# Optimization experiments

Hardware: AMD Instinct MI355X
Metric: run time of the kernel (lower is better)

## Reference

```python
import jax, jax.numpy as jnp
import numpy as np

DIM = 1024; HEADS = 16; DH = DIM // HEADS
BLOCK = 64; NSEL = 8
B = 1; N = 2048
CD = BLOCK * DH   # compress_dim
HID = CD          # mlp_expansion = 1


def setup_inputs():
    key = jax.random.key(0)
    ks = jax.random.split(key, 12)
    def nrm(k, shape, scale=0.02):
        return jax.random.normal(k, shape, dtype=jnp.float32) * scale
    x = jax.random.normal(ks[0], (B, N, DIM), dtype=jnp.float32)
    inv = 1.0 / (10000.0 ** (np.arange(0, DH, 2, dtype=np.float32) / DH))
    ang = np.arange(N, dtype=np.float32)[:, None] * inv[None, :]
    freqs_cis = jnp.asarray(np.stack([np.cos(ang), np.sin(ang)], axis=-1))  # [N, DH/2, 2]
    return {
        'x': x, 'freqs_cis': freqs_cis,
        'Wq': nrm(ks[1], (DIM, DIM)), 'Wk': nrm(ks[2], (DIM, DIM)),
        'Wv': nrm(ks[3], (DIM, DIM)), 'Wo': nrm(ks[4], (DIM, DIM)),
        'pe': nrm(ks[5], (BLOCK, HEADS, DH)),
        'kW1': nrm(ks[6], (CD, HID)), 'kb1': jnp.zeros((HID,), jnp.float32),
        'kW2': nrm(ks[7], (HID, DH)), 'kb2': jnp.zeros((DH,), jnp.float32),
        'vW1': nrm(ks[8], (CD, HID)), 'vb1': jnp.zeros((HID,), jnp.float32),
        'vW2': nrm(ks[9], (HID, DH)), 'vb2': jnp.zeros((DH,), jnp.float32),
        'Wc': nrm(ks[10], (DIM, 2 * HEADS)), 'bc': jnp.zeros((2 * HEADS,), jnp.float32),
    }


def _rope(t, cos, sin):
    # t: [b,n,h,d]; rotate consecutive pairs by per-position angles
    t2 = t.reshape(t.shape[:-1] + (DH // 2, 2))
    tr, ti = t2[..., 0], t2[..., 1]
    c = cos[None, :, None, :]
    s = sin[None, :, None, :]
    out = jnp.stack([tr * c - ti * s, tr * s + ti * c], axis=-1)
    return out.reshape(t.shape)


def reference(x, freqs_cis, Wq, Wk, Wv, Wo, pe, kW1, kb1, kW2, kb2, vW1, vb1, vW2, vb2, Wc, bc):
    b, n, _ = x.shape
    w = n // BLOCK
    scale = DH ** -0.5
    q = (x @ Wq).reshape(b, n, HEADS, DH)
    k = (x @ Wk).reshape(b, n, HEADS, DH)
    v = (x @ Wv).reshape(b, n, HEADS, DH)
    # intra-block PE added only on the compression branch
    kb = k.reshape(b, w, BLOCK, HEADS, DH) + pe[None, None]
    vb = v.reshape(b, w, BLOCK, HEADS, DH) + pe[None, None]

    def compress(blocks, W1, b1, W2, b2):
        h = blocks.transpose(0, 1, 3, 2, 4).reshape(b, w, HEADS, CD)  # b w h (n d)
        h = jax.nn.relu(h @ W1 + b1)
        return h @ W2 + b2  # [b,w,h,dh]

    ck = compress(kb, kW1, kb1, kW2, kb2)
    cv = compress(vb, vW1, vb1, vW2, vb2)
    # compressed attention (no rope on q here, matching the source)
    cscore = jax.nn.softmax(jnp.einsum('bqhd,bkhd->bhqk', q, ck) * scale, axis=-1)  # [b,h,n,w]
    compressed = jnp.einsum('bhqk,bkhd->bqhd', cscore, cv)

    cos, sin = freqs_cis[..., 0], freqs_cis[..., 1]
    sq = _rope(q, cos, sin)
    sk = _rope(k, cos, sin)

    nsel = min(NSEL, w)
    idx = jax.lax.top_k(cscore, nsel)[1]  # [b,h,n,nsel] selected block ids per query
    # dense qk scores, then per-query block gather == gathered sparse attention
    sf = (jnp.einsum('bqhd,bkhd->bhqk', sq, sk) * scale).reshape(b, HEADS, n, w, BLOCK)
    sel = jnp.take_along_axis(sf, idx[..., None], axis=3)  # [b,h,n,nsel,BLOCK]
    probs = jax.nn.softmax(sel.reshape(b, HEADS, n, nsel * BLOCK), axis=-1)
    probs = probs.reshape(b, HEADS, n, nsel, BLOCK)
    # scatter selected-softmax back to full key axis (topk ids are distinct)
    onehot = (idx[..., None] == jnp.arange(w)).astype(probs.dtype)  # [b,h,n,nsel,w]
    full = jnp.einsum('bhqsn,bhqsw->bhqwn', probs, onehot).reshape(b, HEADS, n, n)
    selected = jnp.einsum('bhqk,bkhd->bqhd', full, v)  # sv = v without PE

    gate = jax.nn.sigmoid(x @ Wc + bc).reshape(b, n, 2, HEADS)  # b n (s h) -> b n s h
    y = jnp.einsum('bnsh,sbnhd->bnhd', gate, jnp.stack([compressed, selected]))
    return y.reshape(b, n, DIM) @ Wo
```

## Files before the change

kernel.cpp:

```cpp
#include <hip/hip_runtime.h>
#include <hip/hip_bf16.h>

#define N_TOK   2048
#define DIM     1024
#define HEADS   16
#define DH      64
#define WBLK    32
#define NSEL    8
#define CD      4096

typedef __hip_bfloat16 bf16;
typedef __attribute__((ext_vector_type(8))) short short8;
typedef __attribute__((ext_vector_type(4))) float f32x4;

__device__ __forceinline__ void gll16(const void* g, void* l) {
    __builtin_amdgcn_global_load_lds((const __attribute__((address_space(1))) void*)g,
                                     (__attribute__((address_space(3))) void*)l, 16, 0, 0);
}

template<int PAIRS, int OUT>
__global__ __launch_bounds__(256, 2) void gemm_mfma(
    const bf16* __restrict__ a0, const bf16* __restrict__ a1, const bf16* __restrict__ a2,
    const bf16* __restrict__ b0, const bf16* __restrict__ b1, const bf16* __restrict__ b2,
    const float* __restrict__ bias, float* __restrict__ C,
    bf16* __restrict__ C0, bf16* __restrict__ C1,
    int M, int N, int K, int act)
{
    constexpr int NS = (PAIRS == 6) ? 3 : ((PAIRS >= 3) ? 2 : 1);
    __shared__ __align__(16) bf16 As[3][NS][64][32];
    __shared__ __align__(16) bf16 Bs[3][NS][64][32];

    const int tid = threadIdx.x, lane = tid & 63, wid = tid >> 6;
    const int wr = wid >> 1, wc = wid & 1;
    const int row0 = blockIdx.y * 64, col0 = blockIdx.x * 64;

    const bf16* ap[3] = {a0, a1, a2};
    const bf16* bp[3] = {b0, b1, b2};

    f32x4 acc[2][2];
    #pragma unroll
    for (int mi = 0; mi < 2; ++mi)
        #pragma unroll
        for (int ni = 0; ni < 2; ++ni) acc[mi][ni] = (f32x4){0.f, 0.f, 0.f, 0.f};

    const int lr = lane >> 2;
    const int lc = (((lane & 3) ^ ((lane >> 3) & 3))) * 8;
    const int fo = (((lane >> 4) ^ ((lane >> 1) & 3))) * 8;

    constexpr int pa[6] = {0, 0, 1, 1, 0, 2};
    constexpr int pb[6] = {0, 1, 0, 1, 2, 0};

    auto stage = [&](int buf, int t) {
        const int k0 = t << 5;
        #pragma unroll
        for (int s = 0; s < NS; ++s) {
            gll16(ap[s] + (size_t)(row0 + wid * 16 + lr) * K + k0 + lc, &As[buf][s][wid * 16][0]);
            gll16(bp[s] + (size_t)(col0 + wid * 16 + lr) * K + k0 + lc, &Bs[buf][s][wid * 16][0]);
        }
    };

    const int nt = K >> 5;
    stage(0, 0);
    if (nt > 1) {
        stage(1, 1);
        asm volatile("s_waitcnt vmcnt(%0)" :: "n"(2 * NS) : "memory");
    } else {
        asm volatile("s_waitcnt vmcnt(0)" ::: "memory");
    }
    __builtin_amdgcn_s_barrier();

    for (int t = 0; t < nt; ++t) {
        const int cur = t % 3;

        short8 af[2][NS], bfr[2][NS];
        #pragma unroll
        for (int mi = 0; mi < 2; ++mi)
            #pragma unroll
            for (int s = 0; s < NS; ++s)
                af[mi][s] = *(const short8*)&As[cur][s][wr * 32 + mi * 16 + (lane & 15)][fo];
        #pragma unroll
        for (int ni = 0; ni < 2; ++ni)
            #pragma unroll
            for (int s = 0; s < NS; ++s)
                bfr[ni][s] = *(const short8*)&Bs[cur][s][wc * 32 + ni * 16 + (lane & 15)][fo];

        if (t + 2 < nt) stage((t + 2) % 3, t + 2);

        #pragma unroll
        for (int mi = 0; mi < 2; ++mi)
            #pragma unroll
            for (int ni = 0; ni < 2; ++ni) {
                f32x4 c = acc[mi][ni];
                #pragma unroll
                for (int p = 0; p < PAIRS; ++p)
                    c = __builtin_amdgcn_mfma_f32_16x16x32_bf16(af[mi][pa[p]], bfr[ni][pb[p]], c, 0, 0, 0);
                acc[mi][ni] = c;
            }

        if (t + 1 < nt) {
            if (t + 2 < nt) asm volatile("s_waitcnt vmcnt(%0)" :: "n"(2 * NS) : "memory");
            else            asm volatile("s_waitcnt vmcnt(0)" ::: "memory");
            __builtin_amdgcn_s_barrier();
        }
    }

    #pragma unroll
    for (int mi = 0; mi < 2; ++mi)
        #pragma unroll
        for (int ni = 0; ni < 2; ++ni)
            #pragma unroll
            for (int r = 0; r < 4; ++r) {
                int row = row0 + wr * 32 + mi * 16 + (lane >> 4) * 4 + r;
                int col = col0 + wc * 32 + ni * 16 + (lane & 15);
                float v = acc[mi][ni][r];
                if (bias) v += bias[col];
                if (act == 1) v = fmaxf(v, 0.f);
                if (OUT == 0 || OUT == 3) C[(size_t)row * N + col] = v;
                if (OUT == 2 || OUT == 3) {
                    bf16 hh = __float2bfloat16(v);
                    C0[(size_t)row * N + col] = hh;
                    C1[(size_t)row * N + col] = __float2bfloat16(v - __bfloat162float(hh));
                }
            }
}

template<int KC>
__global__ __launch_bounds__(256, 2) void sk_gemm(
    const bf16* __restrict__ a0, const bf16* __restrict__ a1,
    const bf16* __restrict__ b0, const bf16* __restrict__ b1,
    float* __restrict__ part, int M, int K)
{
    __shared__ __align__(16) bf16 As[3][2][64][32];
    __shared__ __align__(16) bf16 Bs[3][2][64][32];
    const int tid = threadIdx.x, lane = tid & 63, wid = tid >> 6;
    const int wr = wid >> 1, wc = wid & 1;
    const int row0 = blockIdx.x * 64;
    const int kchunk = K / KC;
    const int kbase = blockIdx.y * kchunk;
    const bf16* ap[2] = {a0, a1};
    const bf16* bp[2] = {b0, b1};
    const int lr = lane >> 2;
    const int lc = (((lane & 3) ^ ((lane >> 3) & 3))) * 8;
    const int fo = (((lane >> 4) ^ ((lane >> 1) & 3))) * 8;

    f32x4 acc[2][2];
    #pragma unroll
    for (int mi = 0; mi < 2; ++mi)
        #pragma unroll
        for (int ni = 0; ni < 2; ++ni) acc[mi][ni] = (f32x4){0.f, 0.f, 0.f, 0.f};

    auto stage = [&](int buf, int t) {
        const int k0 = kbase + (t << 5);
        #pragma unroll
        for (int s = 0; s < 2; ++s) {
            gll16(ap[s] + (size_t)(row0 + wid * 16 + lr) * K + k0 + lc, &As[buf][s][wid * 16][0]);
            gll16(bp[s] + (size_t)(wid * 16 + lr) * K + k0 + lc,        &Bs[buf][s][wid * 16][0]);
        }
    };

    const int nt = kchunk >> 5;
    stage(0, 0);
    if (nt > 1) {
        stage(1, 1);
        asm volatile("s_waitcnt vmcnt(4)" ::: "memory");
    } else {
        asm volatile("s_waitcnt vmcnt(0)" ::: "memory");
    }
    __builtin_amdgcn_s_barrier();

    for (int t = 0; t < nt; ++t) {
        const int cur = t % 3;
        short8 af[2][2], bfr[2][2];
        #pragma unroll
        for (int mi = 0; mi < 2; ++mi)
            #pragma unroll
            for (int s = 0; s < 2; ++s)
                af[mi][s] = *(const short8*)&As[cur][s][wr * 32 + mi * 16 + (lane & 15)][fo];
        #pragma unroll
        for (int ni = 0; ni < 2; ++ni)
            #pragma unroll
            for (int s = 0; s < 2; ++s)
                bfr[ni][s] = *(const short8*)&Bs[cur][s][wc * 32 + ni * 16 + (lane & 15)][fo];

        if (t + 2 < nt) stage((t + 2) % 3, t + 2);

        #pragma unroll
        for (int mi = 0; mi < 2; ++mi)
            #pragma unroll
            for (int ni = 0; ni < 2; ++ni) {
                f32x4 c = acc[mi][ni];
                c = __builtin_amdgcn_mfma_f32_16x16x32_bf16(af[mi][0], bfr[ni][0], c, 0, 0, 0);
                c = __builtin_amdgcn_mfma_f32_16x16x32_bf16(af[mi][0], bfr[ni][1], c, 0, 0, 0);
                c = __builtin_amdgcn_mfma_f32_16x16x32_bf16(af[mi][1], bfr[ni][0], c, 0, 0, 0);
                acc[mi][ni] = c;
            }

        if (t + 1 < nt) {
            if (t + 2 < nt) asm volatile("s_waitcnt vmcnt(4)" ::: "memory");
            else            asm volatile("s_waitcnt vmcnt(0)" ::: "memory");
            __builtin_amdgcn_s_barrier();
        }
    }

    #pragma unroll
    for (int mi = 0; mi < 2; ++mi)
        #pragma unroll
        for (int ni = 0; ni < 2; ++ni)
            #pragma unroll
            for (int r = 0; r < 4; ++r) {
                int row = row0 + wr * 32 + mi * 16 + (lane >> 4) * 4 + r;
                int col = wc * 32 + ni * 16 + (lane & 15);
                part[((size_t)blockIdx.y * M + row) * 64 + col] = acc[mi][ni][r];
            }
}

__global__ void skred(const float* __restrict__ part, const float* __restrict__ bias,
                      float* __restrict__ C, bf16* __restrict__ C0, bf16* __restrict__ C1,
                      int M, int KC) {
    int i = blockIdx.x * 256 + threadIdx.x;
    if (i >= M * 64) return;
    float s = bias ? bias[i & 63] : 0.f;
    for (int kc = 0; kc < KC; ++kc) s += part[(size_t)kc * M * 64 + i];
    C[i] = s;
    if (C0) {
        bf16 hh = __float2bfloat16(s);
        C0[i] = hh;
        C1[i] = __float2bfloat16(s - __bfloat162float(hh));
    }
}

__global__ __launch_bounds__(256) void cscore_gemm(const bf16* __restrict__ qs0,
                                                   const bf16* __restrict__ qs1,
                                                   const bf16* __restrict__ ck0,
                                                   const bf16* __restrict__ ck1,
                                                   float* __restrict__ Sc) {
    int h = blockIdx.y;
    int wid = threadIdx.x >> 6, lane = threadIdx.x & 63;
    int q0 = blockIdx.x * 128 + wid * 32;
    const int lr = lane & 15, hc = lane >> 4;

    f32x4 acc[2][2];
    #pragma unroll
    for (int a = 0; a < 2; ++a)
        #pragma unroll
        for (int b = 0; b < 2; ++b) acc[a][b] = (f32x4){0.f, 0.f, 0.f, 0.f};

    short8 av[2][2][2], bv[2][2][2];
    #pragma unroll
    for (int qs_ = 0; qs_ < 2; ++qs_)
        #pragma unroll
        for (int ks = 0; ks < 2; ++ks) {
            size_t off = ((size_t)(q0 + qs_ * 16 + lr) << 10) + (h << 6) + ks * 32 + hc * 8;
            av[qs_][ks][0] = *(const short8*)(qs0 + off);
            av[qs_][ks][1] = *(const short8*)(qs1 + off);
        }
    #pragma unroll
    for (int ws = 0; ws < 2; ++ws)
        #pragma unroll
        for (int ks = 0; ks < 2; ++ks) {
            size_t off = ((size_t)(((ws * 16 + lr) << 4) + h)) * 64 + ks * 32 + hc * 8;
            bv[ws][ks][0] = *(const short8*)(ck0 + off);
            bv[ws][ks][1] = *(const short8*)(ck1 + off);
        }
    #pragma unroll
    for (int qs_ = 0; qs_ < 2; ++qs_)
        #pragma unroll
        for (int ws = 0; ws < 2; ++ws) {
            f32x4 c = acc[qs_][ws];
            #pragma unroll
            for (int ks = 0; ks < 2; ++ks) {
                c = __builtin_amdgcn_mfma_f32_16x16x32_bf16(av[qs_][ks][0], bv[ws][ks][0], c, 0, 0, 0);
                c = __builtin_amdgcn_mfma_f32_16x16x32_bf16(av[qs_][ks][0], bv[ws][ks][1], c, 0, 0, 0);
                c = __builtin_amdgcn_mfma_f32_16x16x32_bf16(av[qs_][ks][1], bv[ws][ks][0], c, 0, 0, 0);
            }
            acc[qs_][ws] = c;
        }
    #pragma unroll
    for (int qs_ = 0; qs_ < 2; ++qs_)
        #pragma unroll
        for (int ws = 0; ws < 2; ++ws)
            #pragma unroll
            for (int r = 0; r < 4; ++r) {
                int q = q0 + qs_ * 16 + hc * 4 + r;
                int w = ws * 16 + lr;
                Sc[((size_t)(h << 11) + q) * 32 + w] = acc[qs_][ws][r] * 0.125f;
            }
}

__global__ __launch_bounds__(256) void ctopk_pv(const float* __restrict__ Sc,
                                                const float* __restrict__ cv,
                                                float* __restrict__ comp,
                                                int* __restrict__ idxb) {
    int item = blockIdx.x * 4 + (threadIdx.x >> 6);
    int lane = threadIdx.x & 63;
    int h = item >> 11, qpos = item & 2047;
    float logit = (lane < 32) ? Sc[(size_t)item * 32 + lane] : -1e30f;
    float m = logit;
    #pragma unroll
    for (int o = 32; o; o >>= 1) m = fmaxf(m, __shfl_xor(m, o));
    float e = (lane < 32) ? expf(logit - m) : 0.f;
    float s = e;
    #pragma unroll
    for (int o = 32; o; o >>= 1) s += __shfl_xor(s, o);
    float inv = 1.f / s;
    float acc = 0.f;
    #pragma unroll 8
    for (int w = 0; w < WBLK; ++w) {
        float pw = __shfl(e, w) * inv;
        acc += pw * cv[(size_t)((w << 4) + h) * 64 + lane];
    }
    comp[(size_t)(qpos << 10) + (h << 6) + lane] = acc;
    int rank = 0;
    #pragma unroll 8
    for (int j = 0; j < WBLK; ++j) {
        float lj = __shfl(logit, j);
        rank += (lj > logit || (lj == logit && j < lane)) ? 1 : 0;
    }
    if (lane < 32 && rank < NSEL) idxb[item * NSEL + rank] = lane;
}

__global__ __launch_bounds__(256) void gate_gemm(const float* __restrict__ x,
                                                 const float* __restrict__ Wc,
                                                 const float* __restrict__ bc,
                                                 float* __restrict__ gate) {
    __shared__ float xr[1024];
    __shared__ float part[8][32];
    int row = blockIdx.x;
    #pragma unroll
    for (int i = 0; i < 4; ++i)
        xr[threadIdx.x + i * 256] = x[(size_t)row * 1024 + threadIdx.x + i * 256];
    __syncthreads();
    int c = threadIdx.x & 31, sl = threadIdx.x >> 5;
    float acc = 0.f;
    for (int k = sl; k < 1024; k += 8) acc += xr[k] * Wc[k * 32 + c];
    part[sl][c] = acc;
    __syncthreads();
    if (sl == 0) {
        float v = bc[c];
        #pragma unroll
        for (int j = 0; j < 8; ++j) v += part[j][c];
        gate[(size_t)row * 32 + c] = 1.f / (1.f + expf(-v));
    }
}

template<int NS>
__global__ __launch_bounds__(256) void tsplit(const float* __restrict__ B,
                                              bf16* __restrict__ t0, bf16* __restrict__ t1,
                                              bf16* __restrict__ t2, int K, int N) {
    __shared__ float tile[32][33];
    int tx = threadIdx.x & 31, ty = threadIdx.x >> 5;
    int bx = blockIdx.x, by = blockIdx.y;
    #pragma unroll
    for (int i = 0; i < 4; ++i)
        tile[ty + i * 8][tx] = B[(size_t)(by * 32 + ty + i * 8) * N + bx * 32 + tx];
    __syncthreads();
    #pragma unroll
    for (int i = 0; i < 4; ++i) {
        int nn = bx * 32 + ty + i * 8;
        int kk = by * 32 + tx;
        float x = tile[tx][ty + i * 8];
        bf16 h = __float2bfloat16(x);
        t0[(size_t)nn * K + kk] = h;
        if (NS >= 2) {
            float r1 = x - __bfloat162float(h);
            bf16 m = __float2bfloat16(r1);
            t1[(size_t)nn * K + kk] = m;
            if (NS == 3) t2[(size_t)nn * K + kk] = __float2bfloat16(r1 - __bfloat162float(m));
        }
    }
}

__global__ void split2_k(const float* __restrict__ s, bf16* __restrict__ d0,
                         bf16* __restrict__ d1, int n) {
    int i = blockIdx.x * 256 + threadIdx.x;
    if (i >= n) return;
    float x = s[i];
    bf16 h = __float2bfloat16(x); d0[i] = h;
    d1[i] = __float2bfloat16(x - __bfloat162float(h));
}

__global__ void build_cmat2(const float* __restrict__ kv, const float* __restrict__ pe,
                            bf16* __restrict__ c0, bf16* __restrict__ c1) {
    int i = blockIdx.x * 256 + threadIdx.x;
    int r = i >> 12, c = i & 4095;
    int w = r >> 4, h = r & 15;
    int pos = c >> 6, d = c & 63;
    float x = kv[(size_t)((w * 64 + pos) << 10) + (h << 6) + d] +
              pe[(size_t)((pos << 4) + h) * 64 + d];
    bf16 hh = __float2bfloat16(x); c0[i] = hh;
    c1[i] = __float2bfloat16(x - __bfloat162float(hh));
}
__global__ void build_cmat1(const float* __restrict__ kv, const float* __restrict__ pe,
                            bf16* __restrict__ c0) {
    int i = blockIdx.x * 256 + threadIdx.x;
    int r = i >> 12, c = i & 4095;
    int w = r >> 4, h = r & 15;
    int pos = c >> 6, d = c & 63;
    float x = kv[(size_t)((w * 64 + pos) << 10) + (h << 6) + d] +
              pe[(size_t)((pos << 4) + h) * 64 + d];
    c0[i] = __float2bfloat16(x);
}
__global__ void build_cmat(const float* __restrict__ kv, const float* __restrict__ pe,
                           float* __restrict__ cmat) {
    int i = blockIdx.x * 256 + threadIdx.x;
    int r = i >> 12, c = i & 4095;
    int w = r >> 4, h = r & 15;
    int pos = c >> 6, d = c & 63;
    cmat[i] = kv[(size_t)((w * 64 + pos) << 10) + (h << 6) + d] +
              pe[(size_t)((pos << 4) + h) * 64 + d];
}

__global__ __launch_bounds__(256) void gemm_skinny64(const float* __restrict__ A,
                                                     const float* __restrict__ B,
                                                     const float* __restrict__ bias,
                                                     float* __restrict__ C, int K) {
    __shared__ float Arow[4096];
    __shared__ float part[4][64];
    int row = blockIdx.x;
    for (int i = threadIdx.x; i < K; i += 256) Arow[i] = A[(size_t)row * K + i];
    __syncthreads();
    int c = threadIdx.x & 63, sl = threadIdx.x >> 6;
    float acc = 0.f;
    for (int k = sl; k < K; k += 4) acc += Arow[k] * B[(size_t)k * 64 + c];
    part[sl][c] = acc;
    __syncthreads();
    if (sl == 0) {
        float v = part[0][c] + part[1][c] + part[2][c] + part[3][c];
        if (bias) v += bias[c];
        C[(size_t)row * 64 + c] = v;
    }
}

__global__ __launch_bounds__(256) void gemm_f32(const float* __restrict__ A,
                                                const float* __restrict__ B,
                                                const float* __restrict__ bias,
                                                float* __restrict__ C,
                                                int M, int N, int K, int act) {
    __shared__ float As[16][65];
    __shared__ float Bs[16][65];
    const int tid  = threadIdx.x;
    const int row0 = blockIdx.y * 64;
    const int col0 = blockIdx.x * 64;
    const int tm = tid >> 4;
    const int tn = tid & 15;

    float acc[4][4];
    #pragma unroll
    for (int i = 0; i < 4; ++i)
        #pragma unroll
        for (int j = 0; j < 4; ++j) acc[i][j] = 0.f;

    const int ar  = tid >> 2;
    const int akq = (tid & 3) << 2;

    for (int k0 = 0; k0 < K; k0 += 16) {
        float4 a4 = make_float4(0.f, 0.f, 0.f, 0.f);
        if (row0 + ar < M)
            a4 = *reinterpret_cast<const float4*>(&A[(size_t)(row0 + ar) * K + k0 + akq]);
        As[akq + 0][ar] = a4.x; As[akq + 1][ar] = a4.y;
        As[akq + 2][ar] = a4.z; As[akq + 3][ar] = a4.w;
        #pragma unroll
        for (int it = 0; it < 4; ++it) {
            int idx = tid + it * 256;
            int kr = idx >> 6, c = idx & 63;
            float bv = 0.f;
            if (col0 + c < N) bv = B[(size_t)(k0 + kr) * N + col0 + c];
            Bs[kr][c] = bv;
        }
        __syncthreads();
        #pragma unroll
        for (int kk = 0; kk < 16; ++kk) {
            float a0 = As[kk][tm * 4 + 0], a1 = As[kk][tm * 4 + 1];
            float a2 = As[kk][tm * 4 + 2], a3 = As[kk][tm * 4 + 3];
            float b0v = Bs[kk][tn * 4 + 0], b1v = Bs[kk][tn * 4 + 1];
            float b2v = Bs[kk][tn * 4 + 2], b3v = Bs[kk][tn * 4 + 3];
            acc[0][0] += a0 * b0v; acc[0][1] += a0 * b1v; acc[0][2] += a0 * b2v; acc[0][3] += a0 * b3v;
            acc[1][0] += a1 * b0v; acc[1][1] += a1 * b1v; acc[1][2] += a1 * b2v; acc[1][3] += a1 * b3v;
            acc[2][0] += a2 * b0v; acc[2][1] += a2 * b1v; acc[2][2] += a2 * b2v; acc[2][3] += a2 * b3v;
            acc[3][0] += a3 * b0v; acc[3][1] += a3 * b1v; acc[3][2] += a3 * b2v; acc[3][3] += a3 * b3v;
        }
        __syncthreads();
    }

    #pragma unroll
    for (int i = 0; i < 4; ++i) {
        int r = row0 + tm * 4 + i;
        if (r >= M) continue;
        #pragma unroll
        for (int j = 0; j < 4; ++j) {
            int cc = col0 + tn * 4 + j;
            if (cc >= N) continue;
            float vv = acc[i][j];
            if (bias) vv += bias[cc];
            if (act == 1) vv = fmaxf(vv, 0.f);
            else if (act == 2) vv = 1.f / (1.f + expf(-vv));
            C[(size_t)r * N + cc] = vv;
        }
    }
}

__global__ __launch_bounds__(256) void cscore_topk(const float* __restrict__ q,
                                                   const float* __restrict__ ck,
                                                   float* __restrict__ cprob,
                                                   int* __restrict__ idxb) {
    int item = blockIdx.x * 4 + (threadIdx.x >> 6);
    int lane = threadIdx.x & 63;
    int h = item >> 11;
    int qpos = item & 2047;
    float qv = q[(size_t)(qpos << 10) + (h << 6) + lane];
    float logit = -1e30f;
    const float scale = 0.125f;
    for (int w = 0; w < WBLK; ++w) {
        float p = qv * ck[(size_t)((w << 4) + h) * 64 + lane];
        #pragma unroll
        for (int o = 32; o; o >>= 1) p += __shfl_xor(p, o);
        if (lane == w) logit = p * scale;
    }
    float m = logit;
    #pragma unroll
    for (int o = 32; o; o >>= 1) m = fmaxf(m, __shfl_xor(m, o));
    float e = (lane < 32) ? expf(logit - m) : 0.f;
    float s = e;
    #pragma unroll
    for (int o = 32; o; o >>= 1) s += __shfl_xor(s, o);
    if (lane < 32) cprob[(size_t)item * WBLK + lane] = e / s;
    float vcur = logit;
    for (int t = 0; t < NSEL; ++t) {
        float bm = vcur; int bi = lane;
        #pragma unroll
        for (int o = 32; o; o >>= 1) {
            float om = __shfl_xor(bm, o); int oi = __shfl_xor(bi, o);
            if (om > bm || (om == bm && oi < bi)) { bm = om; bi = oi; }
        }
        if (lane == 0) idxb[item * NSEL + t] = bi;
        if (lane == bi) vcur = -1e30f;
    }
}
__global__ void compressed_pv(const float* __restrict__ cprob, const float* __restrict__ cv,
                              float* __restrict__ comp) {
    int i = blockIdx.x * 256 + threadIdx.x;
    int qpos = i >> 10; int hd = i & 1023; int h = hd >> 6; int d = hd & 63;
    const float* pr = &cprob[(size_t)(h * N_TOK + qpos) * WBLK];
    float acc = 0.f;
    #pragma unroll
    for (int w = 0; w < WBLK; ++w) acc += pr[w] * cv[(size_t)((w << 4) + h) * 64 + d];
    comp[i] = acc;
}

__global__ void rope_ip(float* __restrict__ q, float* __restrict__ k,
                        const float* __restrict__ fc) {
    int i = blockIdx.x * 256 + threadIdx.x;
    int n = i >> 9; int hp = i & 511; int h = hp >> 5; int p = hp & 31;
    float c = fc[(size_t)(n * 32 + p) * 2];
    float s = fc[(size_t)(n * 32 + p) * 2 + 1];
    size_t base = (size_t)(n << 10) + (h << 6) + (p << 1);
    float qr = q[base], qi = q[base + 1];
    q[base] = qr * c - qi * s; q[base + 1] = qr * s + qi * c;
    float kr = k[base], ki = k[base + 1];
    k[base] = kr * c - ki * s; k[base + 1] = kr * s + ki * c;
}

__global__ void rope_convert_qk(const float* __restrict__ q, const float* __restrict__ k,
                                const float* __restrict__ fc,
                                bf16* __restrict__ qb, bf16* __restrict__ kb) {
    int i = blockIdx.x * 256 + threadIdx.x;
    int n = i >> 9; int hp = i & 511; int h = hp >> 5; int p = hp & 31;
    float c = fc[(size_t)(n * 32 + p) * 2];
    float s = fc[(size_t)(n * 32 + p) * 2 + 1];
    size_t base = (size_t)(n << 10) + (h << 6) + (p << 1);
    float qr = q[base], qi = q[base + 1];
    qb[base]     = __float2bfloat16(0.125f * (qr * c - qi * s));
    qb[base + 1] = __float2bfloat16(0.125f * (qr * s + qi * c));
    float kr = k[base], ki = k[base + 1];
    kb[base]     = __float2bfloat16(kr * c - ki * s);
    kb[base + 1] = __float2bfloat16(kr * s + ki * c);
}

__global__ __launch_bounds__(256) void convert_vT(const float* __restrict__ v,
                                                  bf16* __restrict__ vbT) {
    __shared__ float tile[64][65];
    int h = blockIdx.x;
    int n0 = blockIdx.y * 64;
    int tx = threadIdx.x & 63, ty = threadIdx.x >> 6;
    #pragma unroll
    for (int i = 0; i < 16; ++i)
        tile[ty + 4 * i][tx] = v[(size_t)(n0 + ty + 4 * i) * 1024 + (h << 6) + tx];
    __syncthreads();
    #pragma unroll
    for (int i = 0; i < 16; ++i) {
        int d = ty + 4 * i;
        vbT[((size_t)(h << 6) + d) * 2048 + n0 + tx] = __float2bfloat16(tile[tx][d]);
    }
}

__global__ void zero_counts(int* __restrict__ counts) { counts[threadIdx.x] = 0; }

__global__ void build_lists(const int* __restrict__ idxb, int* __restrict__ counts,
                            int* __restrict__ lists) {
    int i = blockIdx.x * 256 + threadIdx.x;
    int item = i >> 3, t = i & 7;
    int h = item >> 11, q = item & 2047;
    int w = idxb[i];
    int g = h * 32 + w;
    int pos = atomicAdd(&counts[g], 1);
    lists[g * 2048 + pos] = (q << 3) | t;
}

__global__ void convert_qkv(const float* __restrict__ q, const float* __restrict__ k,
                            const float* __restrict__ v, bf16* __restrict__ qb,
                            bf16* __restrict__ kb, bf16* __restrict__ vbT) {
    int i = blockIdx.x * 256 + threadIdx.x;
    qb[i] = __float2bfloat16(0.125f * q[i]);
    kb[i] = __float2bfloat16(k[i]);
    int h = i >> 17, d = (i >> 11) & 63, n = i & 2047;
    vbT[i] = __float2bfloat16(v[(size_t)(n << 10) + (h << 6) + d]);
}

__global__ __launch_bounds__(64) void sel_scores(const bf16* __restrict__ qb,
                                                 const bf16* __restrict__ kb,
                                                 const int* __restrict__ counts,
                                                 const int* __restrict__ lists,
                                                 float* __restrict__ S) {
    int g = blockIdx.x;
    int cnt = counts[g];
    int tile = blockIdx.y;
    if (tile * 32 >= cnt) return;
    int h = g >> 5, w = g & 31;
    int lane = threadIdx.x;
    __shared__ int qt[32];
    __shared__ float st[32][66];
    int nrow = cnt - tile * 32; if (nrow > 32) nrow = 32;
    if (lane < 32) qt[lane] = lists[g * 2048 + tile * 32 + (lane < nrow ? lane : nrow - 1)];
    __syncthreads();
    int lr = lane & 15, hc = lane >> 4;

    f32x4 acc[2][4];
    #pragma unroll
    for (int m = 0; m < 2; ++m)
        #pragma unroll
        for (int gk = 0; gk < 4; ++gk) acc[m][gk] = (f32x4){0.f, 0.f, 0.f, 0.f};

    short8 a[2][2], b[4][2];
    #pragma unroll
    for (int m = 0; m < 2; ++m) {
        int qq = qt[m * 16 + lr] >> 3;
        const bf16* ar = qb + ((size_t)qq << 10) + (h << 6) + hc * 8;
        a[m][0] = *(const short8*)ar;
        a[m][1] = *(const short8*)(ar + 32);
    }
    #pragma unroll
    for (int gk = 0; gk < 4; ++gk) {
        const bf16* kr = kb + ((size_t)((w << 6) + gk * 16 + lr) << 10) + (h << 6) + hc * 8;
        b[gk][0] = *(const short8*)kr;
        b[gk][1] = *(const short8*)(kr + 32);
    }
    #pragma unroll
    for (int m = 0; m < 2; ++m)
        #pragma unroll
        for (int gk = 0; gk < 4; ++gk) {
            acc[m][gk] = __builtin_amdgcn_mfma_f32_16x16x32_bf16(a[m][0], b[gk][0], acc[m][gk], 0, 0, 0);
            acc[m][gk] = __builtin_amdgcn_mfma_f32_16x16x32_bf16(a[m][1], b[gk][1], acc[m][gk], 0, 0, 0);
        }
    #pragma unroll
    for (int m = 0; m < 2; ++m)
        #pragma unroll
        for (int gk = 0; gk < 4; ++gk)
            #pragma unroll
            for (int r = 0; r < 4; ++r)
                st[m * 16 + hc * 4 + r][gk * 16 + lr] = acc[m][gk][r];
    __syncthreads();
    for (int rr = 0; rr < nrow; ++rr) {
        int e = qt[rr]; int qq = e >> 3, t = e & 7;
        S[((size_t)((h << 11) + qq) << 9) + (t << 6) + lane] = st[rr][lane];
    }
}

__global__ __launch_bounds__(256) void sel_softmax(const float* __restrict__ S,
                                                   bf16* __restrict__ P) {
    int item = blockIdx.x * 4 + (threadIdx.x >> 6);
    int lane = threadIdx.x & 63;
    const float* row = S + ((size_t)item << 9);
    float v[8]; float m = -1e30f;
    #pragma unroll
    for (int j = 0; j < 8; ++j) { v[j] = row[(j << 6) + lane]; m = fmaxf(m, v[j]); }
    #pragma unroll
    for (int o = 32; o; o >>= 1) m = fmaxf(m, __shfl_xor(m, o));
    float s = 0.f;
    #pragma unroll
    for (int j = 0; j < 8; ++j) { v[j] = expf(v[j] - m); s += v[j]; }
    #pragma unroll
    for (int o = 32; o; o >>= 1) s += __shfl_xor(s, o);
    float inv = 1.f / s;
    #pragma unroll
    for (int j = 0; j < 8; ++j)
        P[((size_t)item << 9) + (j << 6) + lane] = __float2bfloat16(v[j] * inv);
}

__global__ __launch_bounds__(64) void sel_pv(const bf16* __restrict__ P,
                                             const bf16* __restrict__ vbT,
                                             const int* __restrict__ counts,
                                             const int* __restrict__ lists,
                                             float* __restrict__ Opart) {
    int g = blockIdx.x;
    int cnt = counts[g];
    int tile = blockIdx.y;
    if (tile * 32 >= cnt) return;
    int h = g >> 5, w = g & 31;
    int lane = threadIdx.x;
    __shared__ int qt[32];
    __shared__ float st[32][66];
    int nrow = cnt - tile * 32; if (nrow > 32) nrow = 32;
    if (lane < 32) qt[lane] = lists[g * 2048 + tile * 32 + (lane < nrow ? lane : nrow - 1)];
    __syncthreads();
    int lr = lane & 15, hc = lane >> 4;

    f32x4 acc[2][4];
    #pragma unroll
    for (int m = 0; m < 2; ++m)
        #pragma unroll
        for (int dg = 0; dg < 4; ++dg) acc[m][dg] = (f32x4){0.f, 0.f, 0.f, 0.f};

    short8 a[2][2], b[4][2];
    #pragma unroll
    for (int m = 0; m < 2; ++m) {
        int e = qt[m * 16 + lr]; int qq = e >> 3, t = e & 7;
        const bf16* pr = P + ((size_t)((h << 11) + qq) << 9) + (t << 6) + hc * 8;
        a[m][0] = *(const short8*)pr;
        a[m][1] = *(const short8*)(pr + 32);
    }
    #pragma unroll
    for (int dg = 0; dg < 4; ++dg) {
        const bf16* vr = vbT + ((size_t)((h << 6) + dg * 16 + lr) << 11) + (w << 6) + hc * 8;
        b[dg][0] = *(const short8*)vr;
        b[dg][1] = *(const short8*)(vr + 32);
    }
    #pragma unroll
    for (int m = 0; m < 2; ++m)
        #pragma unroll
        for (int dg = 0; dg < 4; ++dg) {
            acc[m][dg] = __builtin_amdgcn_mfma_f32_16x16x32_bf16(a[m][0], b[dg][0], acc[m][dg], 0, 0, 0);
            acc[m][dg] = __builtin_amdgcn_mfma_f32_16x16x32_bf16(a[m][1], b[dg][1], acc[m][dg], 0, 0, 0);
        }
    #pragma unroll
    for (int m = 0; m < 2; ++m)
        #pragma unroll
        for (int dg = 0; dg < 4; ++dg)
            #pragma unroll
            for (int r = 0; r < 4; ++r)
                st[m * 16 + hc * 4 + r][dg * 16 + lr] = acc[m][dg][r];
    __syncthreads();
    for (int rr = 0; rr < nrow; ++rr) {
        int e = qt[rr]; int qq = e >> 3, t = e & 7;
        Opart[((size_t)((h << 11) + qq) << 9) + (t << 6) + lane] = st[rr][lane];
    }
}

__global__ void sel_combine(const float* __restrict__ Opart, const float* __restrict__ comp,
                            const float* __restrict__ gate, float* __restrict__ y) {
    int i = blockIdx.x * 256 + threadIdx.x;
    int qpos = i >> 10, hd = i & 1023, h = hd >> 6, d = hd & 63;
    size_t base = ((size_t)((h << 11) + qpos) << 9) + d;
    float s = 0.f;
    #pragma unroll
    for (int t = 0; t < 8; ++t) s += Opart[base + (t << 6)];
    float g0 = gate[(size_t)qpos * 32 + h];
    float g1 = gate[(size_t)qpos * 32 + 16 + h];
    y[i] = g0 * comp[i] + g1 * s;
}

__global__ __launch_bounds__(64) void selected_attn(const float* __restrict__ sq,
                                                    const float* __restrict__ sk,
                                                    const float* __restrict__ v,
                                                    const int* __restrict__ idxb,
                                                    const float* __restrict__ comp,
                                                    const float* __restrict__ gate,
                                                    float* __restrict__ y) {
    __shared__ float tile[64][65];
    __shared__ float sqs[64];
    __shared__ float pls[64];
    int item = blockIdx.x;
    int h = item >> 11, qpos = item & 2047;
    int lane = threadIdx.x;
    sqs[lane] = sq[(size_t)(qpos << 10) + (h << 6) + lane];
    int idx[NSEL];
    #pragma unroll
    for (int t = 0; t < NSEL; ++t) idx[t] = idxb[item * NSEL + t];

    const float scale = 0.125f;
    float sc[NSEL];
    float m = -1e30f;
    for (int t = 0; t < NSEL; ++t) {
        int w = idx[t];
        __syncthreads();
        for (int r = 0; r < 64; ++r)
            tile[r][lane] = sk[(size_t)((w << 6) + r) * 1024 + (h << 6) + lane];
        __syncthreads();
        float acc = 0.f;
        #pragma unroll
        for (int d = 0; d < 64; ++d) acc += sqs[d] * tile[lane][d];
        sc[t] = acc * scale;
        m = fmaxf(m, sc[t]);
    }
    #pragma unroll
    for (int o = 32; o; o >>= 1) m = fmaxf(m, __shfl_xor(m, o));
    float p[NSEL];
    float denom = 0.f;
    #pragma unroll
    for (int t = 0; t < NSEL; ++t) { p[t] = expf(sc[t] - m); denom += p[t]; }
    #pragma unroll
    for (int o = 32; o; o >>= 1) denom += __shfl_xor(denom, o);
    float inv = 1.f / denom;

    float acc = 0.f;
    for (int t = 0; t < NSEL; ++t) {
        int w = idx[t];
        __syncthreads();
        for (int r = 0; r < 64; ++r)
            tile[r][lane] = v[(size_t)((w << 6) + r) * 1024 + (h << 6) + lane];
        pls[lane] = p[t];
        __syncthreads();
        #pragma unroll
        for (int j = 0; j < 64; ++j) acc += pls[j] * tile[j][lane];
    }
    acc *= inv;

    float g0 = gate[(size_t)qpos * 32 + h];
    float g1 = gate[(size_t)qpos * 32 + 16 + h];
    size_t o = (size_t)(qpos << 10) + (h << 6) + lane;
    y[o] = g0 * comp[o] + g1 * acc;
}

extern "C" void kernel_launch(void* const* d_in, const int* in_sizes, int n_in,
                              void* d_out, int out_size, void* d_ws, size_t ws_size,
                              hipStream_t stream) {
    const float* x   = (const float*)d_in[0];
    const float* fc  = (const float*)d_in[1];
    const float* Wq  = (const float*)d_in[2];
    const float* Wk  = (const float*)d_in[3];
    const float* Wv  = (const float*)d_in[4];
    const float* Wo  = (const float*)d_in[5];
    const float* pe  = (const float*)d_in[6];
    const float* kW1 = (const float*)d_in[7];
    const float* kb1 = (const float*)d_in[8];
    const float* kW2 = (const float*)d_in[9];
    const float* kb2 = (const float*)d_in[10];
    const float* vW1 = (const float*)d_in[11];
    const float* vb1 = (const float*)d_in[12];
    const float* vW2 = (const float*)d_in[13];
    const float* vb2 = (const float*)d_in[14];
    const float* Wc  = (const float*)d_in[15];
    const float* bc  = (const float*)d_in[16];
    float* out = (float*)d_out;

    char* base = (char*)d_ws;
    size_t off = 0;
    auto alloc = [&](size_t bytes) -> void* {
        void* r = base + off;
        off += (bytes + 255) & ~(size_t)255;
        return r;
    };
    const size_t E2M = 2097152;
    float* q     = (float*)alloc(E2M * 4);
    float* k     = (float*)alloc(E2M * 4);
    float* v     = (float*)alloc(E2M * 4);
    float* gate  = (float*)alloc(N_TOK * 32 * 4);
    float* comp  = (float*)alloc(E2M * 4);
    float* hreg  = (float*)alloc(E2M * 4);
    float* y     = (float*)alloc(E2M * 4);
    float* ck    = (float*)alloc(512 * 64 * 4);
    float* cv    = (float*)alloc(512 * 64 * 4);
    float* cprob = (float*)alloc((size_t)HEADS * N_TOK * WBLK * 4);
    int*   idxb  = (int*)alloc((size_t)HEADS * N_TOK * NSEL * 4);
    bf16* xs0 = (bf16*)alloc(E2M * 2);
    bf16* xs1 = (bf16*)alloc(E2M * 2);
    bf16* WqT0 = (bf16*)alloc((size_t)DIM * DIM * 2);
    bf16* WqT1 = (bf16*)alloc((size_t)DIM * DIM * 2);
    bf16* WkT0 = (bf16*)alloc((size_t)DIM * DIM * 2);
    bf16* WkT1 = (bf16*)alloc((size_t)DIM * DIM * 2);
    bf16* WvT  = (bf16*)alloc((size_t)DIM * DIM * 2);
    bf16* WoT0 = (bf16*)alloc((size_t)DIM * DIM * 2);
    bf16* WoT1 = (bf16*)alloc((size_t)DIM * DIM * 2);
    bf16* kW1T0 = (bf16*)alloc((size_t)CD * CD * 2);
    bf16* kW1T1 = (bf16*)alloc((size_t)CD * CD * 2);
    bf16* vW1T  = (bf16*)alloc((size_t)CD * CD * 2);
    bf16* kW2T0 = (bf16*)alloc((size_t)64 * CD * 2);
    bf16* kW2T1 = (bf16*)alloc((size_t)64 * CD * 2);
    bf16* vW2T0 = (bf16*)alloc((size_t)64 * CD * 2);
    bf16* vW2T1 = (bf16*)alloc((size_t)64 * CD * 2);
    bf16* cm0 = (bf16*)alloc(E2M * 2);
    bf16* cm1 = (bf16*)alloc(E2M * 2);
    bf16* y0  = (bf16*)alloc(E2M * 2);
    bf16* y1  = (bf16*)alloc(E2M * 2);
    int*  counts = (int*)alloc(512 * 4);
    int*  lists  = (int*)alloc((size_t)512 * 2048 * 4);
    bf16* qb     = (bf16*)alloc(E2M * 2);
    bf16* kb     = (bf16*)alloc(E2M * 2);
    bf16* vbT    = (bf16*)alloc(E2M * 2);
    bf16* ck0    = (bf16*)alloc(512 * 64 * 2);
    bf16* ck1    = (bf16*)alloc(512 * 64 * 2);
    bf16* Pbuf   = (bf16*)alloc((size_t)HEADS * N_TOK * 512 * 2);
    bf16*  h0    = (bf16*)hreg;
    bf16*  h1    = h0 + (size_t)512 * CD;
    float* part  = y;
    float* Sc    = y;
    bf16*  qs0   = y0;
    bf16*  qs1   = y1;
    float* S     = (float*)kW1T0;
    bf16*  P     = Pbuf;
    float* Opart = (float*)kW1T0;

    dim3 blk(256);
    if (off <= ws_size) {
        split2_k<<<8192, 256, 0, stream>>>(x, xs0, xs1, (int)E2M);
        tsplit<2><<<dim3(32, 32), blk, 0, stream>>>(Wq, WqT0, WqT1, nullptr, DIM, DIM);
        tsplit<2><<<dim3(32, 32), blk, 0, stream>>>(Wk, WkT0, WkT1, nullptr, DIM, DIM);
        tsplit<1><<<dim3(32, 32), blk, 0, stream>>>(Wv, WvT, nullptr, nullptr, DIM, DIM);
        tsplit<2><<<dim3(32, 32), blk, 0, stream>>>(Wo, WoT0, WoT1, nullptr, DIM, DIM);
        tsplit<2><<<dim3(128, 128), blk, 0, stream>>>(kW1, kW1T0, kW1T1, nullptr, CD, CD);
        tsplit<1><<<dim3(128, 128), blk, 0, stream>>>(vW1, vW1T, nullptr, nullptr, CD, CD);
        tsplit<2><<<dim3(2, 128), blk, 0, stream>>>(kW2, kW2T0, kW2T1, nullptr, CD, 64);
        tsplit<2><<<dim3(2, 128), blk, 0, stream>>>(vW2, vW2T0, vW2T1, nullptr, CD, 64);

        gemm_mfma<4, 3><<<dim3(16, 32), blk, 0, stream>>>(xs0, xs1, nullptr, WqT0, WqT1, nullptr,
                                                          nullptr, q, qs0, qs1, N_TOK, DIM, DIM, 0);
        gemm_mfma<4, 0><<<dim3(16, 32), blk, 0, stream>>>(xs0, xs1, nullptr, WkT0, WkT1, nullptr,
                                                          nullptr, k, nullptr, nullptr, N_TOK, DIM, DIM, 0);
        gemm_mfma<1, 0><<<dim3(16, 32), blk, 0, stream>>>(xs0, nullptr, nullptr, WvT, nullptr, nullptr,
                                                          nullptr, v, nullptr, nullptr, N_TOK, DIM, DIM, 0);
        gate_gemm<<<2048, blk, 0, stream>>>(x, Wc, bc, gate);

        build_cmat2<<<8192, 256, 0, stream>>>(k, pe, cm0, cm1);
        gemm_mfma<3, 2><<<dim3(64, 8), blk, 0, stream>>>(cm0, cm1, nullptr, kW1T0, kW1T1, nullptr,
                                                         kb1, nullptr, h0, h1, 512, CD, CD, 1);
        sk_gemm<64><<<dim3(8, 64), blk, 0, stream>>>(h0, h1, kW2T0, kW2T1, part, 512, CD);
        skred<<<128, 256, 0, stream>>>(part, kb2, ck, ck0, ck1, 512, 64);

        build_cmat1<<<8192, 256, 0, stream>>>(v, pe, cm0);
        gemm_mfma<1, 2><<<dim3(64, 8), blk, 0, stream>>>(cm0, nullptr, nullptr, vW1T, nullptr, nullptr,
                                                         vb1, nullptr, h0, h1, 512, CD, CD, 1);
        sk_gemm<64><<<dim3(8, 64), blk, 0, stream>>>(h0, h1, vW2T0, vW2T1, part, 512, CD);
        skred<<<128, 256, 0, stream>>>(part, vb2, cv, nullptr, nullptr, 512, 64);

        cscore_gemm<<<dim3(16, 16), blk, 0, stream>>>(qs0, qs1, ck0, ck1, Sc);
        ctopk_pv<<<8192, 256, 0, stream>>>(Sc, cv, comp, idxb);

        rope_convert_qk<<<4096, 256, 0, stream>>>(q, k, fc, qb, kb);
        convert_vT<<<dim3(16, 32), blk, 0, stream>>>(v, vbT);

        zero_counts<<<1, 512, 0, stream>>>(counts);
        build_lists<<<1024, 256, 0, stream>>>(idxb, counts, lists);
        sel_scores<<<dim3(512, 64), 64, 0, stream>>>(qb, kb, counts, lists, S);
        sel_softmax<<<8192, 256, 0, stream>>>(S, P);
        sel_pv<<<dim3(512, 64), 64, 0, stream>>>(P, vbT, counts, lists, Opart);
        sel_combine<<<8192, 256, 0, stream>>>(Opart, comp, gate, y);

        split2_k<<<8192, 256, 0, stream>>>(y, y0, y1, (int)E2M);
        gemm_mfma<3, 0><<<dim3(16, 32), blk, 0, stream>>>(y0, y1, nullptr, WoT0, WoT1, nullptr,
                                                          nullptr, out, nullptr, nullptr, N_TOK, DIM, DIM, 0);
    } else {
        char* p = (char*)d_ws;
        float* fq    = (float*)p;               p += E2M * 4;
        float* fk    = (float*)p;               p += E2M * 4;
        float* fv    = (float*)p;               p += E2M * 4;
        float* fgate = (float*)p;               p += N_TOK * 32 * 4;
        float* cmat  = (float*)p;               p += E2M * 4;
        float* hbuf  = (float*)p;               p += E2M * 4;
        float* fck   = (float*)p;               p += 512 * 64 * 4;
        float* fcv   = (float*)p;               p += 512 * 64 * 4;
        float* fcpr  = (float*)p;               p += (size_t)HEADS * N_TOK * WBLK * 4;
        int*   fidx  = (int*)p;
        float* fcomp = cmat;
        float* fy    = hbuf;

        gemm_f32<<<dim3(16, 32), blk, 0, stream>>>(x, Wq, nullptr, fq, N_TOK, DIM, DIM, 0);
        gemm_f32<<<dim3(16, 32), blk, 0, stream>>>(x, Wk, nullptr, fk, N_TOK, DIM, DIM, 0);
        gemm_f32<<<dim3(16, 32), blk, 0, stream>>>(x, Wv, nullptr, fv, N_TOK, DIM, DIM, 0);
        gemm_f32<<<dim3(1, 32),  blk, 0, stream>>>(x, Wc, bc, fgate, N_TOK, 2 * HEADS, DIM, 2);
        build_cmat<<<8192, 256, 0, stream>>>(fk, pe, cmat);
        gemm_f32<<<dim3(64, 8), blk, 0, stream>>>(cmat, kW1, kb1, hbuf, 512, CD, CD, 1);
        gemm_skinny64<<<512, blk, 0, stream>>>(hbuf, kW2, kb2, fck, CD);
        build_cmat<<<8192, 256, 0, stream>>>(fv, pe, cmat);
        gemm_f32<<<dim3(64, 8), blk, 0, stream>>>(cmat, vW1, vb1, hbuf, 512, CD, CD, 1);
        gemm_skinny64<<<512, blk, 0, stream>>>(hbuf, vW2, vb2, fcv, CD);
        cscore_topk<<<8192, 256, 0, stream>>>(fq, fck, fcpr, fidx);
        compressed_pv<<<8192, 256, 0, stream>>>(fcpr, fcv, fcomp);
        rope_ip<<<4096, 256, 0, stream>>>(fq, fk, fc);
        selected_attn<<<32768, 64, 0, stream>>>(fq, fk, fv, fidx, fcomp, fgate, fy);
        gemm_f32<<<dim3(16, 32), blk, 0, stream>>>(fy, Wo, nullptr, out, N_TOK, DIM, DIM, 0);
    }
}
```

Baseline: 571.5 us.

## Fuse cmat building into projection GEMMs and split-K the compression MLP

The PE-add and block-layout conversion for the compression input are moved into the epilogues of the K and V projection GEMMs, which removes the separate build_cmat kernels. The first compression-MLP layer (M=512) now runs through a new 128-row-tile split-K=2 GEMM with a reduction kernel that applies bias, ReLU and the bf16 split, to get more blocks onto the device. The counts zeroing is folded into cscore_gemm, and the bf16 split of y is folded into sel_combine. Together these cut several small launches and full-tensor round trips. The cost is extra partial-sum traffic and an added reduction kernel.

```diff
diff --git a/kernel.cpp b/kernel.cpp
--- a/kernel.cpp
+++ b/kernel.cpp
@@ -24,7 +24,7 @@
     const bf16* __restrict__ b0, const bf16* __restrict__ b1, const bf16* __restrict__ b2,
     const float* __restrict__ bias, float* __restrict__ C,
     bf16* __restrict__ C0, bf16* __restrict__ C1,
-    int M, int N, int K, int act)
+    int M, int N, int K, int act, const float* __restrict__ pe)
 {
     constexpr int NS = (PAIRS == 6) ? 3 : ((PAIRS >= 3) ? 2 : 1);
     __shared__ __align__(16) bf16 As[3][NS][64][32];
@@ -115,13 +115,130 @@
                 float v = acc[mi][ni][r];
                 if (bias) v += bias[col];
                 if (act == 1) v = fmaxf(v, 0.f);
-                if (OUT == 0 || OUT == 3) C[(size_t)row * N + col] = v;
+                if (OUT == 0 || OUT == 3 || OUT == 5 || OUT == 6) C[(size_t)row * N + col] = v;
                 if (OUT == 2 || OUT == 3) {
                     bf16 hh = __float2bfloat16(v);
                     C0[(size_t)row * N + col] = hh;
                     C1[(size_t)row * N + col] = __float2bfloat16(v - __bfloat162float(hh));
                 }
+                if (OUT == 5 || OUT == 6) {
+                    int w_ = row >> 6, pos = row & 63, hh_ = col >> 6, d_ = col & 63;
+                    float xx = v + pe[(size_t)((pos << 4) + hh_) * 64 + d_];
+                    size_t ci = ((size_t)((w_ << 4) + hh_) << 12) + (pos << 6) + d_;
+                    bf16 bb = __float2bfloat16(xx);
+                    C0[ci] = bb;
+                    if (OUT == 5) C1[ci] = __float2bfloat16(xx - __bfloat162float(bb));
+                }
             }
+}
+
+template<int PAIRS>
+__global__ __launch_bounds__(256, 2) void gemm_bigk(
+    const bf16* __restrict__ a0, const bf16* __restrict__ a1,
+    const bf16* __restrict__ b0, const bf16* __restrict__ b1,
+    float* __restrict__ part, int M, int N, int K)
+{
+    constexpr int NS = (PAIRS >= 3) ? 2 : 1;
+    __shared__ __align__(16) bf16 As[3][NS][128][32];
+    __shared__ __align__(16) bf16 Bs[3][NS][64][32];
+
+    const int tid = threadIdx.x, lane = tid & 63, wid = tid >> 6;
+    const int wr = wid >> 1, wc = wid & 1;
+    const int row0 = blockIdx.y * 128, col0 = blockIdx.x * 64;
+    const int kchunk = K >> 1;
+    const int kbase = blockIdx.z * kchunk;
+
+    const bf16* ap[2] = {a0, a1};
+    const bf16* bp[2] = {b0, b1};
+
+    f32x4 acc[4][2];
+    #pragma unroll
+    for (int mi = 0; mi < 4; ++mi)
+        #pragma unroll
+        for (int ni = 0; ni < 2; ++ni) acc[mi][ni] = (f32x4){0.f, 0.f, 0.f, 0.f};
+
+    const int lr = lane >> 2;
+    const int lc = (((lane & 3) ^ ((lane >> 3) & 3))) * 8;
+    const int fo = (((lane >> 4) ^ ((lane >> 1) & 3))) * 8;
+
+    constexpr int pa[3] = {0, 0, 1};
+    constexpr int pb[3] = {0, 1, 0};
+
+    auto stage = [&](int buf, int t) {
+        const int k0 = kbase + (t << 5);
+        #pragma unroll
+        for (int s = 0; s < NS; ++s) {
+            gll16(ap[s] + (size_t)(row0 + wid * 32 + lr) * K + k0 + lc,      &As[buf][s][wid * 32][0]);
+            gll16(ap[s] + (size_t)(row0 + wid * 32 + 16 + lr) * K + k0 + lc, &As[buf][s][wid * 32 + 16][0]);
+            gll16(bp[s] + (size_t)(col0 + wid * 16 + lr) * K + k0 + lc,      &Bs[buf][s][wid * 16][0]);
+        }
+    };
+
+    const int nt = kchunk >> 5;
+    stage(0, 0);
+    if (nt > 1) {
+        stage(1, 1);
+        asm volatile("s_waitcnt vmcnt(%0)" :: "n"(3 * NS) : "memory");
+    } else {
+        asm volatile("s_waitcnt vmcnt(0)" ::: "memory");
+    }
+    __builtin_amdgcn_s_barrier();
+
+    for (int t = 0; t < nt; ++t) {
+        const int cur = t % 3;
+
+        short8 af[4][NS], bfr[2][NS];
+        #pragma unroll
+        for (int mi = 0; mi < 4; ++mi)
+            #pragma unroll
+            for (int s = 0; s < NS; ++s)
+                af[mi][s] = *(const short8*)&As[cur][s][wr * 64 + mi * 16 + (lane & 15)][fo];
+        #pragma unroll
+        for (int ni = 0; ni < 2; ++ni)
+            #pragma unroll
+            for (int s = 0; s < NS; ++s)
+                bfr[ni][s] = *(const short8*)&Bs[cur][s][wc * 32 + ni * 16 + (lane & 15)][fo];
+
+        if (t + 2 < nt) stage((t + 2) % 3, t + 2);
+
+        #pragma unroll
+        for (int mi = 0; mi < 4; ++mi)
+            #pragma unroll
+            for (int ni = 0; ni < 2; ++ni) {
+                f32x4 c = acc[mi][ni];
+                #pragma unroll
+                for (int p = 0; p < PAIRS; ++p)
+                    c = __builtin_amdgcn_mfma_f32_16x16x32_bf16(af[mi][pa[p]], bfr[ni][pb[p]], c, 0, 0, 0);
+                acc[mi][ni] = c;
+            }
+
+        if (t + 1 < nt) {
+            if (t + 2 < nt) asm volatile("s_waitcnt vmcnt(%0)" :: "n"(3 * NS) : "memory");
+            else            asm volatile("s_waitcnt vmcnt(0)" ::: "memory");
+            __builtin_amdgcn_s_barrier();
+        }
+    }
+
+    #pragma unroll
+    for (int mi = 0; mi < 4; ++mi)
+        #pragma unroll
+        for (int ni = 0; ni < 2; ++ni)
+            #pragma unroll
+            for (int r = 0; r < 4; ++r) {
+                int row = row0 + wr * 64 + mi * 16 + (lane >> 4) * 4 + r;
+                int col = col0 + wc * 32 + ni * 16 + (lane & 15);
+                part[((size_t)blockIdx.z * M + row) * N + col] = acc[mi][ni][r];
+            }
+}
+
+__global__ void kredh(const float* __restrict__ part, const float* __restrict__ bias,
+                      bf16* __restrict__ h0, bf16* __restrict__ h1) {
+    int i = blockIdx.x * 256 + threadIdx.x;
+    float s = part[i] + part[(size_t)512 * CD + i] + bias[i & (CD - 1)];
+    s = fmaxf(s, 0.f);
+    bf16 hh = __float2bfloat16(s);
+    h0[i] = hh;
+    h1[i] = __float2bfloat16(s - __bfloat162float(hh));
 }
 
 template<int KC>
@@ -233,7 +350,12 @@
                                                    const bf16* __restrict__ qs1,
                                                    const bf16* __restrict__ ck0,
                                                    const bf16* __restrict__ ck1,
-                                                   float* __restrict__ Sc) {
+                                                   float* __restrict__ Sc,
+                                                   int* __restrict__ counts) {
+    if (blockIdx.x == 0 && blockIdx.y == 0) {
+        counts[threadIdx.x] = 0;
+        counts[threadIdx.x + 256] = 0;
+    }
     int h = blockIdx.y;
     int wid = threadIdx.x >> 6, lane = threadIdx.x & 63;
     int q0 = blockIdx.x * 128 + wid * 32;
@@ -379,27 +501,6 @@
     d1[i] = __float2bfloat16(x - __bfloat162float(h));
 }
 
-__global__ void build_cmat2(const float* __restrict__ kv, const float* __restrict__ pe,
-                            bf16* __restrict__ c0, bf16* __restrict__ c1) {
-    int i = blockIdx.x * 256 + threadIdx.x;
-    int r = i >> 12, c = i & 4095;
-    int w = r >> 4, h = r & 15;
-    int pos = c >> 6, d = c & 63;
-    float x = kv[(size_t)((w * 64 + pos) << 10) + (h << 6) + d] +
-              pe[(size_t)((pos << 4) + h) * 64 + d];
-    bf16 hh = __float2bfloat16(x); c0[i] = hh;
-    c1[i] = __float2bfloat16(x - __bfloat162float(hh));
-}
-__global__ void build_cmat1(const float* __restrict__ kv, const float* __restrict__ pe,
-                            bf16* __restrict__ c0) {
-    int i = blockIdx.x * 256 + threadIdx.x;
-    int r = i >> 12, c = i & 4095;
-    int w = r >> 4, h = r & 15;
-    int pos = c >> 6, d = c & 63;
-    float x = kv[(size_t)((w * 64 + pos) << 10) + (h << 6) + d] +
-              pe[(size_t)((pos << 4) + h) * 64 + d];
-    c0[i] = __float2bfloat16(x);
-}
 __global__ void build_cmat(const float* __restrict__ kv, const float* __restrict__ pe,
                            float* __restrict__ cmat) {
     int i = blockIdx.x * 256 + threadIdx.x;
@@ -593,8 +694,6 @@
     }
 }
 
-__global__ void zero_counts(int* __restrict__ counts) { counts[threadIdx.x] = 0; }
-
 __global__ void build_lists(const int* __restrict__ idxb, int* __restrict__ counts,
                             int* __restrict__ lists) {
     int i = blockIdx.x * 256 + threadIdx.x;
@@ -756,7 +855,8 @@
 }
 
 __global__ void sel_combine(const float* __restrict__ Opart, const float* __restrict__ comp,
-                            const float* __restrict__ gate, float* __restrict__ y) {
+                            const float* __restrict__ gate,
+                            bf16* __restrict__ y0, bf16* __restrict__ y1) {
     int i = blockIdx.x * 256 + threadIdx.x;
     int qpos = i >> 10, hd = i & 1023, h = hd >> 6, d = hd & 63;
     size_t base = ((size_t)((h << 11) + qpos) << 9) + d;
@@ -765,7 +865,10 @@
     for (int t = 0; t < 8; ++t) s += Opart[base + (t << 6)];
     float g0 = gate[(size_t)qpos * 32 + h];
     float g1 = gate[(size_t)qpos * 32 + 16 + h];
-    y[i] = g0 * comp[i] + g1 * s;
+    float val = g0 * comp[i] + g1 * s;
+    bf16 b0 = __float2bfloat16(val);
+    y0[i] = b0;
+    y1[i] = __float2bfloat16(val - __bfloat162float(b0));
 }
 
 __global__ __launch_bounds__(64) void selected_attn(const float* __restrict__ sq,
@@ -889,6 +992,7 @@
     bf16* vW2T1 = (bf16*)alloc((size_t)64 * CD * 2);
     bf16* cm0 = (bf16*)alloc(E2M * 2);
     bf16* cm1 = (bf16*)alloc(E2M * 2);
+    bf16* cmv0 = (bf16*)alloc(E2M * 2);
     bf16* y0  = (bf16*)alloc(E2M * 2);
     bf16* y1  = (bf16*)alloc(E2M * 2);
     int*  counts = (int*)alloc(512 * 4);
@@ -899,15 +1003,16 @@
     bf16* ck0    = (bf16*)alloc(512 * 64 * 2);
     bf16* ck1    = (bf16*)alloc(512 * 64 * 2);
     bf16* Pbuf   = (bf16*)alloc((size_t)HEADS * N_TOK * 512 * 2);
-    bf16*  h0    = (bf16*)hreg;
-    bf16*  h1    = h0 + (size_t)512 * CD;
-    float* part  = y;
-    float* Sc    = y;
-    bf16*  qs0   = y0;
-    bf16*  qs1   = y1;
-    float* S     = (float*)kW1T0;
-    bf16*  P     = Pbuf;
-    float* Opart = (float*)kW1T0;
+    bf16*  h0     = (bf16*)hreg;
+    bf16*  h1     = h0 + (size_t)512 * CD;
+    float* part   = y;
+    float* Sc     = y;
+    bf16*  qs0    = y0;
+    bf16*  qs1    = y1;
+    float* partL1 = (float*)Pbuf;
+    float* S      = (float*)kW1T0;
+    bf16*  P      = Pbuf;
+    float* Opart  = (float*)kW1T0;
 
     dim3 blk(256);
     if (off <= ws_size) {
@@ -922,41 +1027,37 @@
         tsplit<2><<<dim3(2, 128), blk, 0, stream>>>(vW2, vW2T0, vW2T1, nullptr, CD, 64);
 
         gemm_mfma<4, 3><<<dim3(16, 32), blk, 0, stream>>>(xs0, xs1, nullptr, WqT0, WqT1, nullptr,
-                                                          nullptr, q, qs0, qs1, N_TOK, DIM, DIM, 0);
-        gemm_mfma<4, 0><<<dim3(16, 32), blk, 0, stream>>>(xs0, xs1, nullptr, WkT0, WkT1, nullptr,
-                                                          nullptr, k, nullptr, nullptr, N_TOK, DIM, DIM, 0);
-        gemm_mfma<1, 0><<<dim3(16, 32), blk, 0, stream>>>(xs0, nullptr, nullptr, WvT, nullptr, nullptr,
-                                                          nullptr, v, nullptr, nullptr, N_TOK, DIM, DIM, 0);
+                                                          nullptr, q, qs0, qs1, N_TOK, DIM, DIM, 0, nullptr);
+        gemm_mfma<4, 5><<<dim3(16, 32), blk, 0, stream>>>(xs0, xs1, nullptr, WkT0, WkT1, nullptr,
+                                                          nullptr, k, cm0, cm1, N_TOK, DIM, DIM, 0, pe);
+        gemm_mfma<1, 6><<<dim3(16, 32), blk, 0, stream>>>(xs0, nullptr, nullptr, WvT, nullptr, nullptr,
+                                                          nullptr, v, cmv0, nullptr, N_TOK, DIM, DIM, 0, pe);
         gate_gemm<<<2048, blk, 0, stream>>>(x, Wc, bc, gate);
 
-        build_cmat2<<<8192, 256, 0, stream>>>(k, pe, cm0, cm1);
-        gemm_mfma<3, 2><<<dim3(64, 8), blk, 0, stream>>>(cm0, cm1, nullptr, kW1T0, kW1T1, nullptr,
-                                                         kb1, nullptr, h0, h1, 512, CD, CD, 1);
+        gemm_bigk<3><<<dim3(64, 4, 2), blk, 0, stream>>>(cm0, cm1, kW1T0, kW1T1, partL1, 512, CD, CD);
+        kredh<<<8192, 256, 0, stream>>>(partL1, kb1, h0, h1);
         sk_gemm<64><<<dim3(8, 64), blk, 0, stream>>>(h0, h1, kW2T0, kW2T1, part, 512, CD);
         skred<<<128, 256, 0, stream>>>(part, kb2, ck, ck0, ck1, 512, 64);
 
-        build_cmat1<<<8192, 256, 0, stream>>>(v, pe, cm0);
-        gemm_mfma<1, 2><<<dim3(64, 8), blk, 0, stream>>>(cm0, nullptr, nullptr, vW1T, nullptr, nullptr,
-                                                         vb1, nullptr, h0, h1, 512, CD, CD, 1);
+        gemm_bigk<1><<<dim3(64, 4, 2), blk, 0, stream>>>(cmv0, nullptr, vW1T, nullptr, partL1, 512, CD, CD);
+        kredh<<<8192, 256, 0, stream>>>(partL1, vb1, h0, h1);
         sk_gemm<64><<<dim3(8, 64), blk, 0, stream>>>(h0, h1, vW2T0, vW2T1, part, 512, CD);
         skred<<<128, 256, 0, stream>>>(part, vb2, cv, nullptr, nullptr, 512, 64);
 
-        cscore_gemm<<<dim3(16, 16), blk, 0, stream>>>(qs0, qs1, ck0, ck1, Sc);
+        cscore_gemm<<<dim3(16, 16), blk, 0, stream>>>(qs0, qs1, ck0, ck1, Sc, counts);
         ctopk_pv<<<8192, 256, 0, stream>>>(Sc, cv, comp, idxb);
 
         rope_convert_qk<<<4096, 256, 0, stream>>>(q, k, fc, qb, kb);
         convert_vT<<<dim3(16, 32), blk, 0, stream>>>(v, vbT);
 
-        zero_counts<<<1, 512, 0, stream>>>(counts);
         build_lists<<<1024, 256, 0, stream>>>(idxb, counts, lists);
         sel_scores<<<dim3(512, 64), 64, 0, stream>>>(qb, kb, counts, lists, S);
         sel_softmax<<<8192, 256, 0, stream>>>(S, P);
         sel_pv<<<dim3(512, 64), 64, 0, stream>>>(P, vbT, counts, lists, Opart);
-        sel_combine<<<8192, 256, 0, stream>>>(Opart, comp, gate, y);
-
-        split2_k<<<8192, 256, 0, stream>>>(y, y0, y1, (int)E2M);
+        sel_combine<<<8192, 256, 0, stream>>>(Opart, comp, gate, y0, y1);
+
         gemm_mfma<3, 0><<<dim3(16, 32), blk, 0, stream>>>(y0, y1, nullptr, WoT0, WoT1, nullptr,
-                                                          nullptr, out, nullptr, nullptr, N_TOK, DIM, DIM, 0);
+                                                          nullptr, out, nullptr, nullptr, N_TOK, DIM, DIM, 0, nullptr);
     } else {
         char* p = (char*)d_ws;
         float* fq    = (float*)p;               p += E2M * 4;
```

After: 556.6 us. -2.6%, faster.
